# Performance work log

Measured on AMD Instinct MI355X. Metric: run time of the kernel, lower is better.

Reference implementation:

```python
import jax, jax.numpy as jnp
import numpy as np

B, S, D = 2, 2048, 1024
H, HD = 16, 64  # num_heads, hidden_size per head


def setup_inputs() -> dict:
    key = jax.random.key(0)
    ks = jax.random.split(key, 10)
    inp = {
        'queries': jax.random.normal(ks[0], (B, S, D), jnp.float32),
        'keys': jax.random.normal(ks[1], (B, S, D), jnp.float32),
        'values': jax.random.normal(ks[2], (B, S, D), jnp.float32),
        # binary indicator masks (some zeros so renorm guard path is exercised)
        'ind_q': (jax.random.uniform(ks[3], (B, S)) > 0.2).astype(jnp.float32),
        'ind_k': (jax.random.uniform(ks[4], (B, S)) > 0.2).astype(jnp.float32),
        'ind_v': (jax.random.uniform(ks[5], (B, S)) > 0.2).astype(jnp.float32),
        'Wq': jax.random.normal(ks[6], (D, H * HD), jnp.float32) / np.sqrt(D),
        'Wk': jax.random.normal(ks[7], (D, H * HD), jnp.float32) / np.sqrt(D),
        'Wv': jax.random.normal(ks[8], (D, H * HD), jnp.float32) / np.sqrt(D),
        'Wo': jax.random.normal(ks[9], (H * HD, D), jnp.float32) / np.sqrt(H * HD),
    }
    return inp


def reference(queries, keys, values, ind_q, ind_k, ind_v, Wq, Wk, Wv, Wo):
    b, nq, _ = queries.shape
    nk = keys.shape[1]
    # projections -> [B, H, S, HD], masked by indicators
    Q = (queries @ Wq).reshape(b, nq, H, HD).transpose(0, 2, 1, 3) * ind_q[:, None, :, None]
    K = (keys @ Wk).reshape(b, nk, H, HD).transpose(0, 2, 1, 3) * ind_k[:, None, :, None]
    V = (values @ Wv).reshape(b, nk, H, HD).transpose(0, 2, 1, 3) * ind_v[:, None, :, None]
    # scaled dot-product scores, plain softmax over keys
    scores = jnp.einsum('bhqd,bhkd->bhqk', Q, K) / jnp.sqrt(jnp.float32(HD))
    attn = jax.nn.softmax(scores, axis=-1)
    # post-softmax multiplicative key-indicator mask + renormalization with zero-row guard
    attn = attn * ind_k[:, None, None, :]
    denom = jnp.sum(attn, axis=-1, keepdims=True)
    attn = attn / jnp.where(denom == 0.0, 1.0, denom)
    out = jnp.einsum('bhqk,bhkd->bhqd', attn, V)  # [B, H, Q, HD]
    out = out.transpose(0, 2, 1, 3).reshape(b, nq, H * HD)
    return out @ Wo
```

## Files before the change

### kernel.cpp

```cpp
#include <hip/hip_runtime.h>
#include <math.h>

typedef __attribute__((ext_vector_type(8))) short bf16x8;
typedef __attribute__((ext_vector_type(4))) float f32x4;

__device__ __forceinline__ unsigned short f2b(float f) {
    union { float f; unsigned int u; } v; v.f = f;
    unsigned int u = v.u + 0x7FFFu + ((v.u >> 16) & 1u);
    return (unsigned short)(u >> 16);
}

__device__ __forceinline__ f32x4 mfma16(bf16x8 a, bf16x8 b, f32x4 c) {
    return __builtin_amdgcn_mfma_f32_16x16x32_bf16(a, b, c, 0, 0, 0);
}

__device__ __forceinline__ void async_ld16(void* l, const void* g) {
    __builtin_amdgcn_global_load_lds(
        (__attribute__((address_space(1))) void*)g,
        (__attribute__((address_space(3))) void*)l, 16, 0, 0);
}

__device__ __forceinline__ float exp2_hw(float x) {
    float r; asm("v_exp_f32 %0, %1" : "=v"(r) : "v"(x)); return r;
}

__device__ __forceinline__ unsigned int cvtpk_bf16(float a, float b) {
    unsigned int r;
    asm("v_cvt_pk_bf16_f32 %0, %1, %2" : "=v"(r) : "v"(a), "v"(b));
    return r;
}

__global__ __launch_bounds__(256) void prep(
    const float* __restrict__ q, const float* __restrict__ k,
    const float* __restrict__ v, unsigned short* __restrict__ qo,
    unsigned short* __restrict__ ko, unsigned short* __restrict__ vo,
    const float* __restrict__ W0, const float* __restrict__ W1,
    const float* __restrict__ W2, const float* __restrict__ W3,
    unsigned short* __restrict__ T0, unsigned short* __restrict__ T1,
    unsigned short* __restrict__ T2, unsigned short* __restrict__ T3)
{
    __shared__ short Ls[64 * 65];
    const int bid = blockIdx.x;
    const int t = threadIdx.x;
    if (bid < 12288) {
        const int z = bid >> 12, blk = bid & 4095;
        const float* in = (z == 0) ? q : (z == 1) ? k : v;
        unsigned short* out = (z == 0) ? qo : (z == 1) ? ko : vo;
        const int i = (blk * 256 + t) * 4;
        const float4 x = *(const float4*)(in + i);
        ushort4 o; o.x = f2b(x.x); o.y = f2b(x.y); o.z = f2b(x.z); o.w = f2b(x.w);
        *(ushort4*)(out + i) = o;
        return;
    }
    const int r = bid - 12288;
    const int z = r >> 8, rem = r & 255;
    const int k0 = (rem >> 4) * 64, n0 = (rem & 15) * 64;
    const float* W = (z == 0) ? W0 : (z == 1) ? W1 : (z == 2) ? W2 : W3;
    unsigned short* T = (z == 0) ? T0 : (z == 1) ? T1 : (z == 2) ? T2 : T3;
#pragma unroll
    for (int ii = 0; ii < 4; ++ii) {
        const int kl = (t >> 4) + 16 * ii, nl = (t & 15) * 4;
        const float4 vv = *(const float4*)&W[(size_t)(k0 + kl) * 1024 + n0 + nl];
        Ls[kl * 65 + nl + 0] = (short)f2b(vv.x);
        Ls[kl * 65 + nl + 1] = (short)f2b(vv.y);
        Ls[kl * 65 + nl + 2] = (short)f2b(vv.z);
        Ls[kl * 65 + nl + 3] = (short)f2b(vv.w);
    }
    __syncthreads();
#pragma unroll
    for (int ii = 0; ii < 4; ++ii) {
        const int nl = (t >> 4) + 16 * ii, kl = (t & 15) * 4;
        ushort4 o;
        o.x = (unsigned short)Ls[(kl + 0) * 65 + nl];
        o.y = (unsigned short)Ls[(kl + 1) * 65 + nl];
        o.z = (unsigned short)Ls[(kl + 2) * 65 + nl];
        o.w = (unsigned short)Ls[(kl + 3) * 65 + nl];
        *(ushort4*)&T[(size_t)(n0 + nl) * 1024 + k0 + kl] = o;
    }
}

__global__ __launch_bounds__(256) void gemm_proj(
    const unsigned short* __restrict__ qb, const unsigned short* __restrict__ kb,
    const unsigned short* __restrict__ vb,
    const unsigned short* __restrict__ BtAll,
    unsigned short* __restrict__ Qw, unsigned short* __restrict__ Kw,
    unsigned short* __restrict__ Vw,
    const float* __restrict__ iq, const float* __restrict__ ik,
    const float* __restrict__ iv)
{
    const unsigned hw = blockIdx.x;
    const unsigned xcd = hw & 7, j = hw >> 3;
    const unsigned mloc = j / 24, ntg = j - mloc * 24;
    const int mt = (int)(xcd * 4 + mloc);
    const int z = (int)(ntg >> 3), ntl = (int)(ntg & 7);
    const int m0 = mt * 128, n0 = (int)ntg * 128;

    const unsigned short* A = (z == 0) ? qb : (z == 1) ? kb : vb;
    unsigned short* Cw      = (z == 0) ? Qw : (z == 1) ? Kw : Vw;
    const float* msk        = (z == 0) ? iq : (z == 1) ? ik : iv;
    const float scale = (z == 0) ? 0.125f * 1.44269504088896f : 1.0f;

    __shared__ __align__(16) short As[128 * 32];
    __shared__ __align__(16) short Bs[128 * 32];
    __shared__ float maskL[128];
    const int t = threadIdx.x;
    const int w = t >> 6, lane = t & 63, l15 = lane & 15, quad = lane >> 4;
    const int wr = w >> 1, wc = w & 1;
    if (t < 128) maskL[t] = msk[m0 + t] * scale;

    const int srow = lane >> 2, soff = (lane & 3) * 8;

    f32x4 zero4 = {0.f, 0.f, 0.f, 0.f};
    f32x4 acc[4][4];
#pragma unroll
    for (int i = 0; i < 4; ++i)
#pragma unroll
        for (int j2 = 0; j2 < 4; ++j2) acc[i][j2] = zero4;

    for (int k0 = 0; k0 < 1024; k0 += 32) {
        __syncthreads();
#pragma unroll
        for (int i = 0; i < 2; ++i) {
            const int r = 16 * (2 * w + i);
            async_ld16(As + r * 32, A     + (size_t)(m0 + r + srow) * 1024 + k0 + soff);
            async_ld16(Bs + r * 32, BtAll + (size_t)(n0 + r + srow) * 1024 + k0 + soff);
        }
        __syncthreads();
        bf16x8 af[4], bfr[4];
#pragma unroll
        for (int i = 0; i < 4; ++i)
            af[i] = *(const bf16x8*)&As[(64 * wr + 16 * i + l15) * 32 + 8 * quad];
#pragma unroll
        for (int j2 = 0; j2 < 4; ++j2)
            bfr[j2] = *(const bf16x8*)&Bs[(64 * wc + 16 * j2 + l15) * 32 + 8 * quad];
#pragma unroll
        for (int i = 0; i < 4; ++i)
#pragma unroll
            for (int j2 = 0; j2 < 4; ++j2)
                acc[i][j2] = mfma16(af[i], bfr[j2], acc[i][j2]);
    }

    const int h = 2 * ntl + wc;
#pragma unroll
    for (int i = 0; i < 4; ++i)
#pragma unroll
        for (int j2 = 0; j2 < 4; ++j2)
#pragma unroll
            for (int reg = 0; reg < 4; ++reg) {
                const int mloc2 = 64 * wr + 16 * i + 4 * quad + reg;
                const int m = m0 + mloc2;
                const int bb = m >> 11, s = m & 2047;
                const int hd = 16 * j2 + l15;
                Cw[((size_t)(bb * 16 + h) * 2048 + s) * 64 + hd] =
                    f2b(acc[i][j2][reg] * maskL[mloc2]);
            }
}

__global__ __launch_bounds__(256) void gemm_out(
    const unsigned short* __restrict__ A, const unsigned short* __restrict__ Bt,
    float* __restrict__ C)
{
    __shared__ __align__(16) short As[128 * 32];
    __shared__ __align__(16) short Bs[64 * 32];
    const int t = threadIdx.x;
    const int w = t >> 6, lane = t & 63, l15 = lane & 15, quad = lane >> 4;
    const int wr = w >> 1, wc = w & 1;
    const unsigned hw = blockIdx.x;
    const unsigned xcd = hw & 7, j = hw >> 3;
    const unsigned mt = xcd * 4 + (j >> 4);
    const unsigned nt = j & 15;
    const int n0 = nt * 64, m0 = mt * 128;
    const int srow = lane >> 2, soff = (lane & 3) * 8;

    f32x4 zero4 = {0.f, 0.f, 0.f, 0.f};
    f32x4 acc[4][2];
#pragma unroll
    for (int i = 0; i < 4; ++i) { acc[i][0] = zero4; acc[i][1] = zero4; }

    for (int k0 = 0; k0 < 1024; k0 += 32) {
        __syncthreads();
#pragma unroll
        for (int i = 0; i < 2; ++i) {
            const int r = 16 * (2 * w + i);
            async_ld16(As + r * 32, A + (size_t)(m0 + r + srow) * 1024 + k0 + soff);
        }
        async_ld16(Bs + (16 * w) * 32, Bt + (size_t)(n0 + 16 * w + srow) * 1024 + k0 + soff);
        __syncthreads();
        bf16x8 af[4], bfr[2];
#pragma unroll
        for (int i = 0; i < 4; ++i)
            af[i] = *(const bf16x8*)&As[(64 * wr + 16 * i + l15) * 32 + 8 * quad];
#pragma unroll
        for (int jj = 0; jj < 2; ++jj)
            bfr[jj] = *(const bf16x8*)&Bs[(32 * wc + 16 * jj + l15) * 32 + 8 * quad];
#pragma unroll
        for (int i = 0; i < 4; ++i)
#pragma unroll
            for (int jj = 0; jj < 2; ++jj)
                acc[i][jj] = mfma16(af[i], bfr[jj], acc[i][jj]);
    }
#pragma unroll
    for (int i = 0; i < 4; ++i)
#pragma unroll
        for (int jj = 0; jj < 2; ++jj)
#pragma unroll
            for (int reg = 0; reg < 4; ++reg) {
                const int m = m0 + 64 * wr + 16 * i + 4 * quad + reg;
                const int n = n0 + 32 * wc + 16 * jj + l15;
                C[(size_t)m * 1024 + n] = acc[i][jj][reg];
            }
}

#define GST 72

__global__ __launch_bounds__(512, 4) void attn_mfma(
    const unsigned short* __restrict__ Qw, const unsigned short* __restrict__ Kw,
    const unsigned short* __restrict__ Vw, const float* __restrict__ indk,
    unsigned short* __restrict__ AO)
{
    __shared__ __align__(16) short Ks[2][64 * GST];
    __shared__ __align__(16) short Vt[2][64 * GST];
    __shared__ float Bl[2048];
    const int t = threadIdx.x;
    const int w = t >> 6, lane = t & 63, l15 = lane & 15, quad = lane >> 4;
    const unsigned wg = (blockIdx.x & 7) * 64 + (blockIdx.x >> 3);
    const int q0 = (wg & 15) * 128;
    const int h = (wg >> 4) & 15, b = wg >> 8;
    const size_t base = (size_t)(b * 16 + h) * (2048 * 64);
    const unsigned short* Qb = Qw + base + (size_t)q0 * 64;
    const unsigned short* Kb = Kw + base;
    const unsigned short* Vb = Vw + base;

    bf16x8 qf[2];
    qf[0] = *(const bf16x8*)&Qb[(16 * w + l15) * 64 + 8 * quad];
    qf[1] = *(const bf16x8*)&Qb[(16 * w + l15) * 64 + 32 + 8 * quad];

    {
        const float4 bi = *(const float4*)&indk[b * 2048 + t * 4];
        float4 bo;
        bo.x = (bi.x - 1.f) * 1e30f; bo.y = (bi.y - 1.f) * 1e30f;
        bo.z = (bi.z - 1.f) * 1e30f; bo.w = (bi.w - 1.f) * 1e30f;
        *(float4*)&Bl[t * 4] = bo;
    }

    const int skr = t >> 3, skc = (t & 7) * 8;
    const int slr = skr ^ (((skr >> 3) & 1) << 2);
    const int dq = t >> 5, kp2 = (t & 31) * 2;

    bf16x8 kreg;
    ushort4 vreg[2];
    kreg = *(const bf16x8*)&Kb[(size_t)skr * 64 + skc];
    vreg[0] = *(const ushort4*)&Vb[(size_t)kp2 * 64 + 4 * dq];
    vreg[1] = *(const ushort4*)&Vb[(size_t)(kp2 + 1) * 64 + 4 * dq];

    const int u_ = l15 >> 2, a_ = l15 & 3;
    const int krA = 8 * u_ + 4 * (u_ & 1) + a_;
    const int krB = 8 * u_ + 4 * (1 - (u_ & 1)) + a_;

    union { unsigned int u[4]; bf16x8 b; } ones;
    ones.u[0] = 0x3F803F80u; ones.u[1] = 0x3F803F80u;
    ones.u[2] = 0x3F803F80u; ones.u[3] = 0x3F803F80u;

    f32x4 zero4 = {0.f, 0.f, 0.f, 0.f};
    f32x4 oacc[4];
    oacc[0] = zero4; oacc[1] = zero4; oacc[2] = zero4; oacc[3] = zero4;
    f32x4 lacc = zero4;

    for (int c = 0; c < 32; ++c) {
        const int cur = c & 1;
        *(bf16x8*)&Ks[cur][slr * GST + skc] = kreg;
        {
            const unsigned int* v0d = (const unsigned int*)&vreg[0];
            const unsigned int* v1d = (const unsigned int*)&vreg[1];
            *(unsigned int*)&Vt[cur][(4 * dq + 0) * GST + kp2] =
                __builtin_amdgcn_perm(v1d[0], v0d[0], 0x05040100u);
            *(unsigned int*)&Vt[cur][(4 * dq + 1) * GST + kp2] =
                __builtin_amdgcn_perm(v1d[0], v0d[0], 0x07060302u);
            *(unsigned int*)&Vt[cur][(4 * dq + 2) * GST + kp2] =
                __builtin_amdgcn_perm(v1d[1], v0d[1], 0x05040100u);
            *(unsigned int*)&Vt[cur][(4 * dq + 3) * GST + kp2] =
                __builtin_amdgcn_perm(v1d[1], v0d[1], 0x07060302u);
        }
        __syncthreads();
        {
            const int kn = (c < 31 ? c + 1 : 31) * 64;
            kreg = *(const bf16x8*)&Kb[(size_t)(kn + skr) * 64 + skc];
            vreg[0] = *(const ushort4*)&Vb[(size_t)(kn + kp2) * 64 + 4 * dq];
            vreg[1] = *(const ushort4*)&Vb[(size_t)(kn + kp2 + 1) * 64 + 4 * dq];
        }
        const short* KsC = Ks[cur];
        const short* VtC = Vt[cur];
        const float* BlC = Bl + c * 64;

        f32x4 sacc[4];
#pragma unroll
        for (int g = 0; g < 4; ++g) {
            const float4 bv = *(const float4*)&BlC[32 * (g >> 1) + 4 * (g & 1) + 8 * quad];
            sacc[g][0] = bv.x; sacc[g][1] = bv.y; sacc[g][2] = bv.z; sacc[g][3] = bv.w;
        }
        __builtin_amdgcn_s_setprio(1);
#pragma unroll
        for (int ks = 0; ks < 2; ++ks)
#pragma unroll
            for (int g = 0; g < 4; ++g) {
                const int row = 32 * (g >> 1) + ((g & 1) ? krB : krA);
                const bf16x8 kf = *(const bf16x8*)&KsC[row * GST + 32 * ks + 8 * quad];
                sacc[g] = mfma16(kf, qf[ks], sacc[g]);
            }
        __builtin_amdgcn_s_setprio(0);

        unsigned int dw[4][2];
#pragma unroll
        for (int g = 0; g < 4; ++g) {
#pragma unroll
            for (int r = 0; r < 4; ++r) sacc[g][r] = exp2_hw(sacc[g][r]);
            dw[g][0] = cvtpk_bf16(sacc[g][0], sacc[g][1]);
            dw[g][1] = cvtpk_bf16(sacc[g][2], sacc[g][3]);
        }

        __builtin_amdgcn_s_setprio(1);
#pragma unroll
        for (int ks = 0; ks < 2; ++ks) {
            union { unsigned int u[4]; bf16x8 b; } pc;
            pc.u[0] = dw[2 * ks][0];     pc.u[1] = dw[2 * ks][1];
            pc.u[2] = dw[2 * ks + 1][0]; pc.u[3] = dw[2 * ks + 1][1];
#pragma unroll
            for (int nj = 0; nj < 4; ++nj) {
                const bf16x8 vbf = *(const bf16x8*)
                    &VtC[(16 * nj + l15) * GST + 32 * ks + 8 * quad];
                oacc[nj] = mfma16(pc.b, vbf, oacc[nj]);
            }
            lacc = mfma16(pc.b, ones.b, lacc);
        }
        __builtin_amdgcn_s_setprio(0);
    }

    float invr[4];
#pragma unroll
    for (int r = 0; r < 4; ++r)
        invr[r] = (lacc[r] > 0.f) ? 1.f / lacc[r] : 0.f;
#pragma unroll
    for (int nj = 0; nj < 4; ++nj)
#pragma unroll
        for (int r = 0; r < 4; ++r) {
            const int row = q0 + 16 * w + 4 * quad + r;
            AO[(size_t)(b * 2048 + row) * 1024 + h * 64 + 16 * nj + l15] =
                f2b(oacc[nj][r] * invr[r]);
        }
}

extern "C" void kernel_launch(void* const* d_in, const int* in_sizes, int n_in,
                              void* d_out, int out_size, void* d_ws, size_t ws_size,
                              hipStream_t stream) {
    const float* q  = (const float*)d_in[0];
    const float* k  = (const float*)d_in[1];
    const float* v  = (const float*)d_in[2];
    const float* iq = (const float*)d_in[3];
    const float* ik = (const float*)d_in[4];
    const float* iv = (const float*)d_in[5];
    const float* Wq = (const float*)d_in[6];
    const float* Wk = (const float*)d_in[7];
    const float* Wv = (const float*)d_in[8];
    const float* Wo = (const float*)d_in[9];
    float* out = (float*)d_out;
    unsigned short* ws = (unsigned short*)d_ws;

    const size_t M1 = 1048576;
    unsigned short* qb  = ws;
    unsigned short* kb  = ws + 4  * M1;
    unsigned short* vb  = ws + 8  * M1;
    unsigned short* Wqt = ws + 12 * M1;
    unsigned short* Wkt = ws + 13 * M1;
    unsigned short* Wvt = ws + 14 * M1;
    unsigned short* Wot = ws + 15 * M1;
    unsigned short* Qw  = ws + 16 * M1;
    unsigned short* Kw  = ws + 20 * M1;
    unsigned short* Vw  = ws + 24 * M1;
    unsigned short* AO  = ws + 28 * M1;

    prep<<<dim3(13312, 1, 1), dim3(256), 0, stream>>>(
        q, k, v, qb, kb, vb, Wq, Wk, Wv, Wo, Wqt, Wkt, Wvt, Wot);
    gemm_proj<<<dim3(768, 1, 1), dim3(256), 0, stream>>>(
        qb, kb, vb, Wqt, Qw, Kw, Vw, iq, ik, iv);
    attn_mfma<<<dim3(512, 1, 1), dim3(512), 0, stream>>>(Qw, Kw, Vw, ik, AO);
    gemm_out<<<dim3(512, 1, 1), dim3(256), 0, stream>>>(AO, Wot, out);
}
```

Before: 220.8 us.

## Double K-tile depth to 64 with XOR-swizzled LDS layout in projection GEMMs

Both the QKV projection GEMM and the output GEMM now stage 64-wide K slices per iteration instead of 32. This halves the number of barrier pairs and loop iterations. The shared-memory tiles use an XOR swizzle on 16-byte column chunks so that fragment reads avoid bank conflicts. s_setprio is raised around the MFMA bursts so that waves issuing matrix ops get scheduling priority. LDS use per block doubles, which may reduce occupancy.

```diff
diff --git a/kernel.cpp b/kernel.cpp
--- a/kernel.cpp
+++ b/kernel.cpp
@@ -100,15 +100,17 @@
     const float* msk        = (z == 0) ? iq : (z == 1) ? ik : iv;
     const float scale = (z == 0) ? 0.125f * 1.44269504088896f : 1.0f;
 
-    __shared__ __align__(16) short As[128 * 32];
-    __shared__ __align__(16) short Bs[128 * 32];
+    __shared__ __align__(16) short As[128 * 64];
+    __shared__ __align__(16) short Bs[128 * 64];
     __shared__ float maskL[128];
     const int t = threadIdx.x;
     const int w = t >> 6, lane = t & 63, l15 = lane & 15, quad = lane >> 4;
     const int wr = w >> 1, wc = w & 1;
     if (t < 128) maskL[t] = msk[m0 + t] * scale;
 
-    const int srow = lane >> 2, soff = (lane & 3) * 8;
+    const int srow = t >> 3;
+    const int scol = ((t & 7) ^ ((t >> 3) & 7)) * 8;
+    const int l7 = l15 & 7;
 
     f32x4 zero4 = {0.f, 0.f, 0.f, 0.f};
     f32x4 acc[4][4];
@@ -117,27 +119,33 @@
 #pragma unroll
         for (int j2 = 0; j2 < 4; ++j2) acc[i][j2] = zero4;
 
-    for (int k0 = 0; k0 < 1024; k0 += 32) {
+    for (int k0 = 0; k0 < 1024; k0 += 64) {
         __syncthreads();
 #pragma unroll
-        for (int i = 0; i < 2; ++i) {
-            const int r = 16 * (2 * w + i);
-            async_ld16(As + r * 32, A     + (size_t)(m0 + r + srow) * 1024 + k0 + soff);
-            async_ld16(Bs + r * 32, BtAll + (size_t)(n0 + r + srow) * 1024 + k0 + soff);
+        for (int u = 0; u < 4; ++u) {
+            const int r = u * 32 + srow;
+            async_ld16(As + u * 2048 + t * 8, A     + (size_t)(m0 + r) * 1024 + k0 + scol);
+            async_ld16(Bs + u * 2048 + t * 8, BtAll + (size_t)(n0 + r) * 1024 + k0 + scol);
         }
         __syncthreads();
-        bf16x8 af[4], bfr[4];
-#pragma unroll
-        for (int i = 0; i < 4; ++i)
-            af[i] = *(const bf16x8*)&As[(64 * wr + 16 * i + l15) * 32 + 8 * quad];
-#pragma unroll
-        for (int j2 = 0; j2 < 4; ++j2)
-            bfr[j2] = *(const bf16x8*)&Bs[(64 * wc + 16 * j2 + l15) * 32 + 8 * quad];
-#pragma unroll
-        for (int i = 0; i < 4; ++i)
+#pragma unroll
+        for (int ks = 0; ks < 2; ++ks) {
+            const int cb = ((4 * ks + quad) ^ l7) * 8;
+            bf16x8 af[4], bfr[4];
+#pragma unroll
+            for (int i = 0; i < 4; ++i)
+                af[i] = *(const bf16x8*)&As[(64 * wr + 16 * i + l15) * 64 + cb];
 #pragma unroll
             for (int j2 = 0; j2 < 4; ++j2)
-                acc[i][j2] = mfma16(af[i], bfr[j2], acc[i][j2]);
+                bfr[j2] = *(const bf16x8*)&Bs[(64 * wc + 16 * j2 + l15) * 64 + cb];
+            __builtin_amdgcn_s_setprio(1);
+#pragma unroll
+            for (int i = 0; i < 4; ++i)
+#pragma unroll
+                for (int j2 = 0; j2 < 4; ++j2)
+                    acc[i][j2] = mfma16(af[i], bfr[j2], acc[i][j2]);
+            __builtin_amdgcn_s_setprio(0);
+        }
     }
 
     const int h = 2 * ntl + wc;
@@ -160,8 +168,8 @@
     const unsigned short* __restrict__ A, const unsigned short* __restrict__ Bt,
     float* __restrict__ C)
 {
-    __shared__ __align__(16) short As[128 * 32];
-    __shared__ __align__(16) short Bs[64 * 32];
+    __shared__ __align__(16) short As[128 * 64];
+    __shared__ __align__(16) short Bs[64 * 64];
     const int t = threadIdx.x;
     const int w = t >> 6, lane = t & 63, l15 = lane & 15, quad = lane >> 4;
     const int wr = w >> 1, wc = w & 1;
@@ -170,34 +178,43 @@
     const unsigned mt = xcd * 4 + (j >> 4);
     const unsigned nt = j & 15;
     const int n0 = nt * 64, m0 = mt * 128;
-    const int srow = lane >> 2, soff = (lane & 3) * 8;
+
+    const int srow = t >> 3;
+    const int scol = ((t & 7) ^ ((t >> 3) & 7)) * 8;
+    const int l7 = l15 & 7;
 
     f32x4 zero4 = {0.f, 0.f, 0.f, 0.f};
     f32x4 acc[4][2];
 #pragma unroll
     for (int i = 0; i < 4; ++i) { acc[i][0] = zero4; acc[i][1] = zero4; }
 
-    for (int k0 = 0; k0 < 1024; k0 += 32) {
+    for (int k0 = 0; k0 < 1024; k0 += 64) {
         __syncthreads();
 #pragma unroll
-        for (int i = 0; i < 2; ++i) {
-            const int r = 16 * (2 * w + i);
-            async_ld16(As + r * 32, A + (size_t)(m0 + r + srow) * 1024 + k0 + soff);
-        }
-        async_ld16(Bs + (16 * w) * 32, Bt + (size_t)(n0 + 16 * w + srow) * 1024 + k0 + soff);
+        for (int u = 0; u < 4; ++u)
+            async_ld16(As + u * 2048 + t * 8, A + (size_t)(m0 + u * 32 + srow) * 1024 + k0 + scol);
+#pragma unroll
+        for (int u = 0; u < 2; ++u)
+            async_ld16(Bs + u * 2048 + t * 8, Bt + (size_t)(n0 + u * 32 + srow) * 1024 + k0 + scol);
         __syncthreads();
-        bf16x8 af[4], bfr[2];
-#pragma unroll
-        for (int i = 0; i < 4; ++i)
-            af[i] = *(const bf16x8*)&As[(64 * wr + 16 * i + l15) * 32 + 8 * quad];
-#pragma unroll
-        for (int jj = 0; jj < 2; ++jj)
-            bfr[jj] = *(const bf16x8*)&Bs[(32 * wc + 16 * jj + l15) * 32 + 8 * quad];
-#pragma unroll
-        for (int i = 0; i < 4; ++i)
+#pragma unroll
+        for (int ks = 0; ks < 2; ++ks) {
+            const int cb = ((4 * ks + quad) ^ l7) * 8;
+            bf16x8 af[4], bfr[2];
+#pragma unroll
+            for (int i = 0; i < 4; ++i)
+                af[i] = *(const bf16x8*)&As[(64 * wr + 16 * i + l15) * 64 + cb];
 #pragma unroll
             for (int jj = 0; jj < 2; ++jj)
-                acc[i][jj] = mfma16(af[i], bfr[jj], acc[i][jj]);
+                bfr[jj] = *(const bf16x8*)&Bs[(32 * wc + 16 * jj + l15) * 64 + cb];
+            __builtin_amdgcn_s_setprio(1);
+#pragma unroll
+            for (int i = 0; i < 4; ++i)
+#pragma unroll
+                for (int jj = 0; jj < 2; ++jj)
+                    acc[i][jj] = mfma16(af[i], bfr[jj], acc[i][jj]);
+            __builtin_amdgcn_s_setprio(0);
+        }
     }
 #pragma unroll
     for (int i = 0; i < 4; ++i)
```

Result: faster. 215.4 us, median of 3 (-2.4%).
